# Performance work log

Measured on AMD Instinct MI355X. Metric: run time of the kernel, lower is better.

## Reference

```python
import jax, jax.numpy as jnp
import numpy as np

N, D = 8192, 128

def setup_inputs() -> dict:
    key = jax.random.key(0)
    kq, kk, kv = jax.random.split(key, 3)
    query = jax.random.normal(kq, (N, D), dtype=jnp.float32)
    key_t = jax.random.normal(kk, (N, D), dtype=jnp.float32)
    value = jax.random.normal(kv, (N, D), dtype=jnp.float32)
    return {"query": query, "key": key_t, "value": value}

def reference(query, key, value):
    # FlashAttention-2 online softmax over blocks is mathematically exact
    # softmax attention: out = softmax(Q K^T / sqrt(d)) V, no mask.
    d = query.shape[-1]
    scale = 1.0 / jnp.sqrt(jnp.asarray(d, dtype=query.dtype))
    scores = jnp.einsum('qd,kd->qk', query, key) * scale  # [n, n]
    probs = jax.nn.softmax(scores, axis=-1)
    return jnp.einsum('qk,kd->qd', probs, value)  # [n, d]
```

## Files before the change

### kernel.cpp

```cpp
#include <hip/hip_runtime.h>
#include <hip/hip_bf16.h>

#define ATTN_N 8192
#define ATTN_D 128
#define TKEYS 32
#define NTILES (ATTN_N / TKEYS)
#define TILE_ELEMS (TKEYS * ATTN_D)
#define QROWS 128
#define SPLITK 8
#define KTPB (NTILES / SPLITK)
#define NBUF 4

typedef __bf16 bf16_t;
typedef bf16_t bf16x2 __attribute__((ext_vector_type(2)));
typedef bf16_t bf16x8 __attribute__((ext_vector_type(8)));
typedef float f32x4 __attribute__((ext_vector_type(4)));

#if __has_builtin(__builtin_amdgcn_exp2f)
#define EXP2(x) __builtin_amdgcn_exp2f(x)
#else
#define EXP2(x) __expf((x) * 0.6931471805599453f)
#endif

__device__ __forceinline__ void dma16(const bf16_t* g, bf16_t* l) {
  __builtin_amdgcn_global_load_lds(
      (const __attribute__((address_space(1))) void*)g,
      (__attribute__((address_space(3))) void*)l, 16, 0, 0);
}

__global__ void prep_kernel(const float* __restrict__ q,
                            const float* __restrict__ k,
                            const float* __restrict__ v,
                            bf16_t* __restrict__ qb,
                            bf16_t* __restrict__ kswz,
                            bf16_t* __restrict__ vtswz) {
  __shared__ bf16_t tile[64][72];
  const int bk = blockIdx.x;
  const int bd = blockIdx.y;
  const int t = threadIdx.x;
  const float sc = 0.12751744f;

  const int row_l = t >> 2;
  const int key = bk * 64 + row_l;

#pragma unroll
  for (int u = 0; u < 2; ++u) {
    const int j = bd * 8 + (t & 3) * 2 + u;
    const float4* qs = (const float4*)(q + (size_t)key * ATTN_D + j * 8);
    const float4* ks = (const float4*)(k + (size_t)key * ATTN_D + j * 8);
    float4 a0 = qs[0], a1 = qs[1];
    float4 b0 = ks[0], b1 = ks[1];
    bf16x8 qo, ko;
    qo[0] = (bf16_t)(a0.x * sc); qo[1] = (bf16_t)(a0.y * sc);
    qo[2] = (bf16_t)(a0.z * sc); qo[3] = (bf16_t)(a0.w * sc);
    qo[4] = (bf16_t)(a1.x * sc); qo[5] = (bf16_t)(a1.y * sc);
    qo[6] = (bf16_t)(a1.z * sc); qo[7] = (bf16_t)(a1.w * sc);
    ko[0] = (bf16_t)b0.x; ko[1] = (bf16_t)b0.y;
    ko[2] = (bf16_t)b0.z; ko[3] = (bf16_t)b0.w;
    ko[4] = (bf16_t)b1.x; ko[5] = (bf16_t)b1.y;
    ko[6] = (bf16_t)b1.z; ko[7] = (bf16_t)b1.w;
    *(bf16x8*)(qb + (size_t)key * ATTN_D + j * 8) = qo;
    *(bf16x8*)(kswz + (size_t)key * ATTN_D + ((j ^ (key & 15)) * 8)) = ko;
  }

  {
    const float* src = v + (size_t)key * ATTN_D + bd * 64 + (t & 3) * 16;
#pragma unroll
    for (int u = 0; u < 4; ++u) {
      float4 a = ((const float4*)src)[u];
      tile[row_l][(t & 3) * 16 + u * 4 + 0] = (bf16_t)a.x;
      tile[row_l][(t & 3) * 16 + u * 4 + 1] = (bf16_t)a.y;
      tile[row_l][(t & 3) * 16 + u * 4 + 2] = (bf16_t)a.z;
      tile[row_l][(t & 3) * 16 + u * 4 + 3] = (bf16_t)a.w;
    }
  }
  __syncthreads();
  {
    const int d_l = t >> 2;
    const int d = bd * 64 + d_l;
    const int cq = t & 3;
#pragma unroll
    for (int h = 0; h < 2; ++h) {
      bf16x8 o;
#pragma unroll
      for (int j = 0; j < 8; ++j) {
        const int kl_ = h * 32 + cq * 4 + (j >> 1) + 16 * (j & 1);
        o[j] = tile[kl_][d_l];
      }
      *(bf16x8*)(vtswz + (size_t)(2 * bk + h) * TILE_ELEMS + d * TKEYS +
                 ((cq ^ ((d >> 1) & 3)) * 8)) = o;
    }
  }
}

__global__ __launch_bounds__(256, 4) void flash_attn_kernel(
    const bf16_t* __restrict__ qb, const bf16_t* __restrict__ kswz,
    const bf16_t* __restrict__ vtswz, float* __restrict__ partO,
    float* __restrict__ partL) {
  __shared__ __align__(16) bf16_t KV[NBUF][2][TILE_ELEMS];
  __shared__ __align__(16) bf16_t Ps[4][32][40];

  const int t = threadIdx.x;
  const int w = t >> 6;
  const int lane = t & 63;
  const int quad = lane >> 4;
  const int col = lane & 15;
  const int blk = blockIdx.x;
  const int qg = blk >> 3;
  const int kh = blk & 7;
  const int q0 = qg * QROWS;
  const int ktbase = kh * KTPB;
  const int stg = ((blk >> 3) & 3) * 8;

  int offK[4][2], offV[8];
#pragma unroll
  for (int c = 0; c < 4; ++c)
#pragma unroll
    for (int ni = 0; ni < 2; ++ni)
      offK[c][ni] = (ni * 16 + col) * ATTN_D + (((c * 4 + quad) ^ col) * 8);
#pragma unroll
  for (int ds = 0; ds < 8; ++ds)
    offV[ds] = (ds * 16 + col) * TKEYS + ((quad ^ ((col >> 1) & 3)) * 8);

  bf16x8 aq[2][4];
#pragma unroll
  for (int mi = 0; mi < 2; ++mi) {
    const int row = q0 + w * 32 + mi * 16 + col;
#pragma unroll
    for (int c = 0; c < 4; ++c)
      aq[mi][c] = *(const bf16x8*)(qb + (size_t)row * ATTN_D + c * 32 + quad * 8);
  }

  f32x4 oacc[2][8];
#pragma unroll
  for (int mi = 0; mi < 2; ++mi)
#pragma unroll
    for (int i = 0; i < 8; ++i) oacc[mi][i] = (f32x4){0.f, 0.f, 0.f, 0.f};
  float l_part[2][4] = {{0.f, 0.f, 0.f, 0.f}, {0.f, 0.f, 0.f, 0.f}};

#pragma unroll
  for (int pt = 0; pt < 3; ++pt) {
    const int kt = ktbase + ((stg + pt) & (KTPB - 1));
#pragma unroll
    for (int u = 0; u < 2; ++u) {
      dma16(kswz + (size_t)kt * TILE_ELEMS + t * 8 + u * 2048,
            &KV[pt][0][t * 8 + u * 2048]);
      dma16(vtswz + (size_t)kt * TILE_ELEMS + t * 8 + u * 2048,
            &KV[pt][1][t * 8 + u * 2048]);
    }
  }
  asm volatile("s_waitcnt vmcnt(8)" ::: "memory");
  __builtin_amdgcn_s_barrier();

  for (int it = 0; it < KTPB; ++it) {
    const int buf = it & (NBUF - 1);
    if (it + 3 < KTPB) {
      const int nt = ktbase + ((stg + it + 3) & (KTPB - 1));
      const int nb = (it + 3) & (NBUF - 1);
#pragma unroll
      for (int u = 0; u < 2; ++u) {
        dma16(kswz + (size_t)nt * TILE_ELEMS + t * 8 + u * 2048,
              &KV[nb][0][t * 8 + u * 2048]);
        dma16(vtswz + (size_t)nt * TILE_ELEMS + t * 8 + u * 2048,
              &KV[nb][1][t * 8 + u * 2048]);
      }
    }
    const bf16_t* Kb = KV[buf][0];
    const bf16_t* Vb = KV[buf][1];

    f32x4 s[2][2];
#pragma unroll
    for (int mi = 0; mi < 2; ++mi)
#pragma unroll
      for (int ni = 0; ni < 2; ++ni) s[mi][ni] = (f32x4){0.f, 0.f, 0.f, 0.f};
    __builtin_amdgcn_s_setprio(1);
#pragma unroll
    for (int c = 0; c < 4; ++c) {
      bf16x8 b0 = *(const bf16x8*)(Kb + offK[c][0]);
      bf16x8 b1 = *(const bf16x8*)(Kb + offK[c][1]);
      s[0][0] = __builtin_amdgcn_mfma_f32_16x16x32_bf16(aq[0][c], b0, s[0][0], 0, 0, 0);
      s[1][0] = __builtin_amdgcn_mfma_f32_16x16x32_bf16(aq[1][c], b0, s[1][0], 0, 0, 0);
      s[0][1] = __builtin_amdgcn_mfma_f32_16x16x32_bf16(aq[0][c], b1, s[0][1], 0, 0, 0);
      s[1][1] = __builtin_amdgcn_mfma_f32_16x16x32_bf16(aq[1][c], b1, s[1][1], 0, 0, 0);
    }
    __builtin_amdgcn_s_setprio(0);

#pragma unroll
    for (int mi = 0; mi < 2; ++mi)
#pragma unroll
      for (int r = 0; r < 4; ++r) {
        float p0 = EXP2(s[mi][0][r]);
        float p1 = EXP2(s[mi][1][r]);
        l_part[mi][r] += p0 + p1;
        *(bf16x2*)&Ps[w][mi * 16 + quad * 4 + r][col * 2] =
            (bf16x2){(bf16_t)p0, (bf16_t)p1};
      }

    bf16x8 ap0 = *(const bf16x8*)&Ps[w][col][quad * 8];
    bf16x8 ap1 = *(const bf16x8*)&Ps[w][16 + col][quad * 8];
    __builtin_amdgcn_s_setprio(1);
#pragma unroll
    for (int ds = 0; ds < 8; ++ds) {
      bf16x8 bv = *(const bf16x8*)(Vb + offV[ds]);
      oacc[0][ds] = __builtin_amdgcn_mfma_f32_16x16x32_bf16(ap0, bv, oacc[0][ds], 0, 0, 0);
      oacc[1][ds] = __builtin_amdgcn_mfma_f32_16x16x32_bf16(ap1, bv, oacc[1][ds], 0, 0, 0);
    }
    __builtin_amdgcn_s_setprio(0);

    if (it + 3 < KTPB) {
      asm volatile("s_waitcnt vmcnt(8)" ::: "memory");
      __builtin_amdgcn_s_barrier();
    } else if (it + 2 < KTPB) {
      asm volatile("s_waitcnt vmcnt(4)" ::: "memory");
      __builtin_amdgcn_s_barrier();
    } else if (it + 1 < KTPB) {
      asm volatile("s_waitcnt vmcnt(0)" ::: "memory");
      __builtin_amdgcn_s_barrier();
    }
  }

#pragma unroll
  for (int mi = 0; mi < 2; ++mi)
#pragma unroll
    for (int r = 0; r < 4; ++r) {
      float v = l_part[mi][r];
#pragma unroll
      for (int off = 1; off < 16; off <<= 1)
        v += __shfl_xor(v, off, 64);
      if (col == 0)
        partL[(size_t)blk * QROWS + w * 32 + mi * 16 + quad * 4 + r] = v;
    }

  {
    float* dst = partO + ((size_t)blk * QROWS + w * 32) * ATTN_D;
#pragma unroll
    for (int mi = 0; mi < 2; ++mi)
#pragma unroll
      for (int ds = 0; ds < 8; ++ds)
#pragma unroll
        for (int r = 0; r < 4; ++r)
          dst[(mi * 16 + quad * 4 + r) * ATTN_D + ds * 16 + col] = oacc[mi][ds][r];
  }
}

__global__ void merge_kernel(const float* __restrict__ partO,
                             const float* __restrict__ partL,
                             float* __restrict__ out) {
  const int idx = blockIdx.x * blockDim.x + threadIdx.x;
  const int row = idx >> 5;
  const int gi = row >> 7;
  const int rl = row & 127;
  const int li = rl * 32 + (idx & 31);
  float L = 0.f;
  float4 acc = {0.f, 0.f, 0.f, 0.f};
#pragma unroll
  for (int i = 0; i < 8; ++i) {
    const size_t b = (size_t)(8 * gi + i);
    L += partL[b * QROWS + rl];
    float4 a = ((const float4*)(partO + b * (QROWS * ATTN_D)))[li];
    acc.x += a.x; acc.y += a.y; acc.z += a.z; acc.w += a.w;
  }
  const float invL = 1.0f / L;
  float4 o;
  o.x = acc.x * invL; o.y = acc.y * invL;
  o.z = acc.z * invL; o.w = acc.w * invL;
  ((float4*)out)[idx] = o;
}

extern "C" void kernel_launch(void* const* d_in, const int* in_sizes, int n_in,
                              void* d_out, int out_size, void* d_ws, size_t ws_size,
                              hipStream_t stream) {
  const float* q = (const float*)d_in[0];
  const float* k = (const float*)d_in[1];
  const float* v = (const float*)d_in[2];
  float* out = (float*)d_out;

  bf16_t* qb = (bf16_t*)d_ws;
  bf16_t* kswz = qb + (size_t)ATTN_N * ATTN_D;
  bf16_t* vtswz = kswz + (size_t)ATTN_N * ATTN_D;
  float* partO = (float*)(vtswz + (size_t)ATTN_N * ATTN_D);
  float* partL = partO + (size_t)512 * QROWS * ATTN_D;

  prep_kernel<<<dim3(ATTN_N / 64, 2), 256, 0, stream>>>(q, k, v, qb, kswz, vtswz);
  flash_attn_kernel<<<512, 256, 0, stream>>>(qb, kswz, vtswz, partO, partL);
  merge_kernel<<<(ATTN_N * ATTN_D / 4) / 256, 256, 0, stream>>>(partO, partL, out);
}
```

Baseline: 112.5 us.

## Compute transposed scores to keep P in registers, drop LDS round-trip

Swaps the MFMA operands in the QK^T step so each lane holds scores for one query row across keys. That register layout matches the A operand of the PV MFMA, so P is packed into bf16x8 directly in registers instead of being written to and reread from shared memory. The V transpose permutation in the prep kernel is changed to match the new key ordering, and the row-sum reduction now needs only two shuffles. Launch bounds are lowered from 4 to 2 blocks per SM, which allows more registers per thread but may reduce occupancy.

Measured after the change: 105.2 us. 6.5% less time.

```diff
diff --git a/kernel.cpp b/kernel.cpp
--- a/kernel.cpp
+++ b/kernel.cpp
@@ -12,7 +12,6 @@
 #define NBUF 4
 
 typedef __bf16 bf16_t;
-typedef bf16_t bf16x2 __attribute__((ext_vector_type(2)));
 typedef bf16_t bf16x8 __attribute__((ext_vector_type(8)));
 typedef float f32x4 __attribute__((ext_vector_type(4)));
 
@@ -84,7 +83,7 @@
       bf16x8 o;
 #pragma unroll
       for (int j = 0; j < 8; ++j) {
-        const int kl_ = h * 32 + cq * 4 + (j >> 1) + 16 * (j & 1);
+        const int kl_ = h * 32 + ((j & 4) << 2) + 4 * cq + (j & 3);
         o[j] = tile[kl_][d_l];
       }
       *(bf16x8*)(vtswz + (size_t)(2 * bk + h) * TILE_ELEMS + d * TKEYS +
@@ -93,12 +92,11 @@
   }
 }
 
-__global__ __launch_bounds__(256, 4) void flash_attn_kernel(
+__global__ __launch_bounds__(256, 2) void flash_attn_kernel(
     const bf16_t* __restrict__ qb, const bf16_t* __restrict__ kswz,
     const bf16_t* __restrict__ vtswz, float* __restrict__ partO,
     float* __restrict__ partL) {
   __shared__ __align__(16) bf16_t KV[NBUF][2][TILE_ELEMS];
-  __shared__ __align__(16) bf16_t Ps[4][32][40];
 
   const int t = threadIdx.x;
   const int w = t >> 6;
@@ -116,27 +114,27 @@
 #pragma unroll
   for (int c = 0; c < 4; ++c)
 #pragma unroll
-    for (int ni = 0; ni < 2; ++ni)
-      offK[c][ni] = (ni * 16 + col) * ATTN_D + (((c * 4 + quad) ^ col) * 8);
+    for (int ks = 0; ks < 2; ++ks)
+      offK[c][ks] = (ks * 16 + col) * ATTN_D + (((c * 4 + quad) ^ col) * 8);
 #pragma unroll
   for (int ds = 0; ds < 8; ++ds)
     offV[ds] = (ds * 16 + col) * TKEYS + ((quad ^ ((col >> 1) & 3)) * 8);
 
   bf16x8 aq[2][4];
 #pragma unroll
-  for (int mi = 0; mi < 2; ++mi) {
-    const int row = q0 + w * 32 + mi * 16 + col;
+  for (int qs = 0; qs < 2; ++qs) {
+    const int row = q0 + w * 32 + qs * 16 + col;
 #pragma unroll
     for (int c = 0; c < 4; ++c)
-      aq[mi][c] = *(const bf16x8*)(qb + (size_t)row * ATTN_D + c * 32 + quad * 8);
+      aq[qs][c] = *(const bf16x8*)(qb + (size_t)row * ATTN_D + c * 32 + quad * 8);
   }
 
   f32x4 oacc[2][8];
 #pragma unroll
-  for (int mi = 0; mi < 2; ++mi)
-#pragma unroll
-    for (int i = 0; i < 8; ++i) oacc[mi][i] = (f32x4){0.f, 0.f, 0.f, 0.f};
-  float l_part[2][4] = {{0.f, 0.f, 0.f, 0.f}, {0.f, 0.f, 0.f, 0.f}};
+  for (int qs = 0; qs < 2; ++qs)
+#pragma unroll
+    for (int i = 0; i < 8; ++i) oacc[qs][i] = (f32x4){0.f, 0.f, 0.f, 0.f};
+  float l_part[2] = {0.f, 0.f};
 
 #pragma unroll
   for (int pt = 0; pt < 3; ++pt) {
@@ -170,40 +168,41 @@
 
     f32x4 s[2][2];
 #pragma unroll
-    for (int mi = 0; mi < 2; ++mi)
-#pragma unroll
-      for (int ni = 0; ni < 2; ++ni) s[mi][ni] = (f32x4){0.f, 0.f, 0.f, 0.f};
+    for (int ks = 0; ks < 2; ++ks)
+#pragma unroll
+      for (int qs = 0; qs < 2; ++qs) s[ks][qs] = (f32x4){0.f, 0.f, 0.f, 0.f};
     __builtin_amdgcn_s_setprio(1);
 #pragma unroll
     for (int c = 0; c < 4; ++c) {
-      bf16x8 b0 = *(const bf16x8*)(Kb + offK[c][0]);
-      bf16x8 b1 = *(const bf16x8*)(Kb + offK[c][1]);
-      s[0][0] = __builtin_amdgcn_mfma_f32_16x16x32_bf16(aq[0][c], b0, s[0][0], 0, 0, 0);
-      s[1][0] = __builtin_amdgcn_mfma_f32_16x16x32_bf16(aq[1][c], b0, s[1][0], 0, 0, 0);
-      s[0][1] = __builtin_amdgcn_mfma_f32_16x16x32_bf16(aq[0][c], b1, s[0][1], 0, 0, 0);
-      s[1][1] = __builtin_amdgcn_mfma_f32_16x16x32_bf16(aq[1][c], b1, s[1][1], 0, 0, 0);
+      bf16x8 k0 = *(const bf16x8*)(Kb + offK[c][0]);
+      bf16x8 k1 = *(const bf16x8*)(Kb + offK[c][1]);
+      s[0][0] = __builtin_amdgcn_mfma_f32_16x16x32_bf16(k0, aq[0][c], s[0][0], 0, 0, 0);
+      s[0][1] = __builtin_amdgcn_mfma_f32_16x16x32_bf16(k0, aq[1][c], s[0][1], 0, 0, 0);
+      s[1][0] = __builtin_amdgcn_mfma_f32_16x16x32_bf16(k1, aq[0][c], s[1][0], 0, 0, 0);
+      s[1][1] = __builtin_amdgcn_mfma_f32_16x16x32_bf16(k1, aq[1][c], s[1][1], 0, 0, 0);
     }
     __builtin_amdgcn_s_setprio(0);
 
-#pragma unroll
-    for (int mi = 0; mi < 2; ++mi)
-#pragma unroll
-      for (int r = 0; r < 4; ++r) {
-        float p0 = EXP2(s[mi][0][r]);
-        float p1 = EXP2(s[mi][1][r]);
-        l_part[mi][r] += p0 + p1;
-        *(bf16x2*)&Ps[w][mi * 16 + quad * 4 + r][col * 2] =
-            (bf16x2){(bf16_t)p0, (bf16_t)p1};
-      }
-
-    bf16x8 ap0 = *(const bf16x8*)&Ps[w][col][quad * 8];
-    bf16x8 ap1 = *(const bf16x8*)&Ps[w][16 + col][quad * 8];
+    bf16x8 ap[2];
+#pragma unroll
+    for (int qs = 0; qs < 2; ++qs) {
+      float pa0 = EXP2(s[0][qs][0]), pa1 = EXP2(s[0][qs][1]);
+      float pa2 = EXP2(s[0][qs][2]), pa3 = EXP2(s[0][qs][3]);
+      float pb0 = EXP2(s[1][qs][0]), pb1 = EXP2(s[1][qs][1]);
+      float pb2 = EXP2(s[1][qs][2]), pb3 = EXP2(s[1][qs][3]);
+      l_part[qs] += (pa0 + pa1 + pa2 + pa3) + (pb0 + pb1 + pb2 + pb3);
+      ap[qs][0] = (bf16_t)pa0; ap[qs][1] = (bf16_t)pa1;
+      ap[qs][2] = (bf16_t)pa2; ap[qs][3] = (bf16_t)pa3;
+      ap[qs][4] = (bf16_t)pb0; ap[qs][5] = (bf16_t)pb1;
+      ap[qs][6] = (bf16_t)pb2; ap[qs][7] = (bf16_t)pb3;
+    }
+
     __builtin_amdgcn_s_setprio(1);
 #pragma unroll
     for (int ds = 0; ds < 8; ++ds) {
       bf16x8 bv = *(const bf16x8*)(Vb + offV[ds]);
-      oacc[0][ds] = __builtin_amdgcn_mfma_f32_16x16x32_bf16(ap0, bv, oacc[0][ds], 0, 0, 0);
-      oacc[1][ds] = __builtin_amdgcn_mfma_f32_16x16x32_bf16(ap1, bv, oacc[1][ds], 0, 0, 0);
+      oacc[0][ds] = __builtin_amdgcn_mfma_f32_16x16x32_bf16(ap[0], bv, oacc[0][ds], 0, 0, 0);
+      oacc[1][ds] = __builtin_amdgcn_mfma_f32_16x16x32_bf16(ap[1], bv, oacc[1][ds], 0, 0, 0);
     }
     __builtin_amdgcn_s_setprio(0);
 
@@ -220,26 +219,23 @@
   }
 
 #pragma unroll
-  for (int mi = 0; mi < 2; ++mi)
-#pragma unroll
-    for (int r = 0; r < 4; ++r) {
-      float v = l_part[mi][r];
-#pragma unroll
-      for (int off = 1; off < 16; off <<= 1)
-        v += __shfl_xor(v, off, 64);
-      if (col == 0)
-        partL[(size_t)blk * QROWS + w * 32 + mi * 16 + quad * 4 + r] = v;
-    }
+  for (int qs = 0; qs < 2; ++qs) {
+    float v = l_part[qs];
+    v += __shfl_xor(v, 16, 64);
+    v += __shfl_xor(v, 32, 64);
+    if (quad == 0)
+      partL[(size_t)blk * QROWS + w * 32 + qs * 16 + col] = v;
+  }
 
   {
     float* dst = partO + ((size_t)blk * QROWS + w * 32) * ATTN_D;
 #pragma unroll
-    for (int mi = 0; mi < 2; ++mi)
+    for (int qs = 0; qs < 2; ++qs)
 #pragma unroll
       for (int ds = 0; ds < 8; ++ds)
 #pragma unroll
         for (int r = 0; r < 4; ++r)
-          dst[(mi * 16 + quad * 4 + r) * ATTN_D + ds * 16 + col] = oacc[mi][ds][r];
+          dst[(qs * 16 + quad * 4 + r) * ATTN_D + ds * 16 + col] = oacc[qs][ds][r];
   }
 }
 
```
